# Performance work log

Hardware: AMD Instinct MI355X
Metric: run time of the kernel (lower is better)

Reference implementation:

```python
import jax, jax.numpy as jnp
import numpy as np

B, L, C, H = 16, 680, 1024, 16
PATCH_NUMS = [1, 4, 9, 16, 25, 36, 64, 100, 169, 256]  # per-scale token counts, sum == L
MAX_SCALE_LOG = float(np.log(100.0))


def setup_inputs() -> dict:
    key = jax.random.key(0)
    ks = jax.random.split(key, 4)
    return {
        "x": jax.random.normal(ks[0], (B, L, C), jnp.float32),
        "patch_nums": jnp.asarray(PATCH_NUMS, jnp.int32),
        "mat_qkv_w": (jax.random.normal(ks[1], (3 * C, C), jnp.float32) * 0.02),
        "q_bias": jnp.zeros((C,), jnp.float32),
        "v_bias": jnp.zeros((C,), jnp.float32),
        "scale_log": jnp.full((1, H, 1, 1), np.log(4.0), jnp.float32),
        "proj_w": (jax.random.normal(ks[2], (C, C), jnp.float32) * 0.02),
        "proj_b": jnp.zeros((C,), jnp.float32),
    }


def _l2norm(t):
    # F.normalize(dim=-1): x / max(||x||_2, eps)
    n = jnp.sqrt(jnp.sum(t * t, axis=-1, keepdims=True))
    return t / jnp.maximum(n, 1e-12)


def reference(x, patch_nums, mat_qkv_w, q_bias, v_bias, scale_log, proj_w, proj_b):
    b, l, c = x.shape
    h = scale_log.shape[1]
    d = c // h
    # fused QKV linear with bias = cat(q_bias, zeros, v_bias)
    bias = jnp.concatenate([q_bias, jnp.zeros_like(q_bias), v_bias])
    qkv = (x @ mat_qkv_w.T + bias).reshape(b, l, 3, h, d)
    q, k, v = qkv[:, :, 0], qkv[:, :, 1], qkv[:, :, 2]  # [B, L, H, D]
    # attn_l2_norm path: scale=1, learned per-head multiplier on normalized q
    scale_mul = jnp.exp(jnp.minimum(scale_log, MAX_SCALE_LOG)).transpose(0, 2, 1, 3)  # (1,1,H,1)
    q = _l2norm(q) * scale_mul
    k = _l2norm(k)
    # training path: block-diagonal varlen attention, one block per scale
    pn = np.asarray(patch_nums).tolist()  # static scale schedule
    outs, start = [], 0
    for ln in pn:
        qs = q[:, start:start + ln]
        ks_ = k[:, start:start + ln]
        vs = v[:, start:start + ln]
        s = jnp.einsum("bihd,bjhd->bhij", qs, ks_)  # softmax_scale = 1
        a = jax.nn.softmax(s, axis=-1)
        outs.append(jnp.einsum("bhij,bjhd->bihd", a, vs))
        start += ln
    oup = jnp.concatenate(outs, axis=1).reshape(b, l, c)
    return oup @ proj_w.T + proj_b
```

## Files before the change

### kernel.cpp

```cpp
#include <hip/hip_runtime.h>

typedef __attribute__((ext_vector_type(8))) short bf16x8;
typedef __attribute__((ext_vector_type(4))) float f32x4;

#define Hh   16
#define Ll   680
#define Cc   1024
#define Bb   16
#define NSEG 10
#define LPAD 720

__device__ __forceinline__ unsigned short f32_bf16(float f) {
  union { float f; unsigned int u; } x; x.f = f;
  unsigned int r = x.u + 0x7FFFu + ((x.u >> 16) & 1u);
  return (unsigned short)(r >> 16);
}
__device__ __forceinline__ float bf16_f32(unsigned short u) {
  union { unsigned int u; float f; } x; x.u = ((unsigned int)u) << 16;
  return x.f;
}

__device__ __forceinline__ void async_copy16(const unsigned short* g, unsigned short* l) {
  __builtin_amdgcn_global_load_lds(
      (const __attribute__((address_space(1))) unsigned int*)g,
      (__attribute__((address_space(3))) unsigned int*)l, 16, 0, 0);
}

__device__ __constant__ int c_start2[11] = {0,1,5,14,30,55,91,155,255,424,680};
__device__ __constant__ int c_ps[NSEG]   = {0,8,16,32,48,80,120,184,288,464};
__device__ __constant__ int c_seg[16]    = {0,1,2,3,4,5,6,7,7,8,8,8,9,9,9,9};
__device__ __constant__ int c_tile0[16]  = {0,0,0,0,0,0,0,0,4,0,4,8,0,4,8,12};
__device__ __constant__ int c_len[NSEG]  = {1,4,9,16,25,36,64,100,169,256};

struct PlTab { unsigned short v[Ll]; };
constexpr PlTab make_pl() {
  PlTab t{};
  int starts[11] = {0,1,5,14,30,55,91,155,255,424,680};
  int ps[10]     = {0,8,16,32,48,80,120,184,288,464};
  for (int s = 0; s < 10; ++s)
    for (int l = starts[s]; l < starts[s + 1]; ++l)
      t.v[l] = (unsigned short)(l - starts[s] + ps[s]);
  return t;
}
__device__ __constant__ PlTab c_plt = make_pl();

__global__ __launch_bounds__(256) void conv_kernel(const float* __restrict__ src,
                                                   unsigned short* __restrict__ dst, int n) {
  int i = (blockIdx.x * 256 + threadIdx.x) * 4;
  if (i + 3 < n) {
    float4 v = *reinterpret_cast<const float4*>(src + i);
    ushort4 o;
    o.x = f32_bf16(v.x); o.y = f32_bf16(v.y); o.z = f32_bf16(v.z); o.w = f32_bf16(v.w);
    *reinterpret_cast<ushort4*>(dst + i) = o;
  }
}

__device__ __forceinline__ void stage_ab(const unsigned short* __restrict__ A,
                                         const unsigned short* __restrict__ Bm,
                                         unsigned short* __restrict__ As,
                                         unsigned short* __restrict__ Bs,
                                         int m0, int n0, int k0, int t, int wbase) {
#pragma unroll
  for (int i = 0; i < 2; ++i) {
    int c = i * 512 + t;
    int r = c >> 3;
    int part = (c & 7) ^ (r & 7);
    async_copy16(A + (size_t)(m0 + r) * 1024 + k0 + part * 8,
                 As + (size_t)(i * 512 + wbase) * 8);
  }
#pragma unroll
  for (int i = 0; i < 4; ++i) {
    int c = i * 512 + t;
    int r = c >> 3;
    int part = (c & 7) ^ (r & 7);
    async_copy16(Bm + (size_t)(n0 + r) * 1024 + k0 + part * 8,
                 Bs + (size_t)(i * 512 + wbase) * 8);
  }
}

__global__ __launch_bounds__(512, 2) void gemm_qkv(const unsigned short* __restrict__ A,
                                                   const unsigned short* __restrict__ Bm,
                                                   const float* __restrict__ qb,
                                                   const float* __restrict__ vb,
                                                   unsigned short* __restrict__ qn,
                                                   unsigned short* __restrict__ kn,
                                                   unsigned short* __restrict__ vtb) {
  __shared__ __align__(16) unsigned short lds[2][24576];
  const int t = threadIdx.x;
  const int lane = t & 63, w = t >> 6;
  const int col = lane & 15, quad = lane >> 4;
  const int wm = (w & 1) * 64, wn = (w >> 1) * 64;
  const int m0 = blockIdx.y * 128, n0 = blockIdx.x * 256;
  const int wbase = w * 64;

  f32x4 acc[4][4];
#pragma unroll
  for (int i = 0; i < 4; ++i)
#pragma unroll
    for (int j = 0; j < 4; ++j)
#pragma unroll
      for (int r = 0; r < 4; ++r) acc[i][j][r] = 0.f;

  stage_ab(A, Bm, lds[0], lds[0] + 8192, m0, n0, 0, t, wbase);
  stage_ab(A, Bm, lds[1], lds[1] + 8192, m0, n0, 64, t, wbase);
  asm volatile("s_waitcnt vmcnt(6)" ::: "memory");
  __builtin_amdgcn_s_barrier();
  __builtin_amdgcn_sched_barrier(0);

  for (int tt = 0; tt < 16; ++tt) {
    unsigned short* As = lds[tt & 1];
    unsigned short* Bs = lds[tt & 1] + 8192;
    bf16x8 bf[4][2], af[2][2];

#pragma unroll
    for (int ni = 0; ni < 4; ++ni) {
      int row = wn + ni * 16 + col;
#pragma unroll
      for (int kq = 0; kq < 2; ++kq)
        bf[ni][kq] = *reinterpret_cast<const bf16x8*>(
            &Bs[(row * 8 + ((kq * 4 + quad) ^ (col & 7))) * 8]);
    }
#pragma unroll
    for (int mi = 0; mi < 2; ++mi) {
      int row = wm + mi * 16 + col;
#pragma unroll
      for (int kq = 0; kq < 2; ++kq)
        af[mi][kq] = *reinterpret_cast<const bf16x8*>(
            &As[(row * 8 + ((kq * 4 + quad) ^ (col & 7))) * 8]);
    }
    __builtin_amdgcn_s_setprio(1);
#pragma unroll
    for (int mi = 0; mi < 2; ++mi)
#pragma unroll
      for (int ni = 0; ni < 4; ++ni)
#pragma unroll
        for (int kq = 0; kq < 2; ++kq)
          acc[mi][ni] = __builtin_amdgcn_mfma_f32_16x16x32_bf16(af[mi][kq], bf[ni][kq],
                                                                acc[mi][ni], 0, 0, 0);
    __builtin_amdgcn_s_setprio(0);
    __builtin_amdgcn_s_barrier();

#pragma unroll
    for (int mi = 0; mi < 2; ++mi) {
      int row = wm + (2 + mi) * 16 + col;
#pragma unroll
      for (int kq = 0; kq < 2; ++kq)
        af[mi][kq] = *reinterpret_cast<const bf16x8*>(
            &As[(row * 8 + ((kq * 4 + quad) ^ (col & 7))) * 8]);
    }
    __builtin_amdgcn_s_setprio(1);
#pragma unroll
    for (int mi = 0; mi < 2; ++mi)
#pragma unroll
      for (int ni = 0; ni < 4; ++ni)
#pragma unroll
        for (int kq = 0; kq < 2; ++kq)
          acc[2 + mi][ni] = __builtin_amdgcn_mfma_f32_16x16x32_bf16(af[mi][kq], bf[ni][kq],
                                                                    acc[2 + mi][ni], 0, 0, 0);
    __builtin_amdgcn_s_setprio(0);
    __builtin_amdgcn_s_barrier();

    if (tt < 14) {
      stage_ab(A, Bm, lds[tt & 1], lds[tt & 1] + 8192, m0, n0, (tt + 2) * 64, t, wbase);
      asm volatile("s_waitcnt vmcnt(6)" ::: "memory");
      __builtin_amdgcn_s_barrier();
      __builtin_amdgcn_sched_barrier(0);
    } else if (tt == 14) {
      asm volatile("s_waitcnt vmcnt(0)" ::: "memory");
      __builtin_amdgcn_s_barrier();
      __builtin_amdgcn_sched_barrier(0);
    }
  }

  const int nbase = n0 + wn;
  const int field = nbase >> 10;
  const int h = (nbase >> 6) & 15;

  if (field < 2) {
    float scl[4][4];
    if (field == 1) {
#pragma unroll
      for (int mi = 0; mi < 4; ++mi)
#pragma unroll
        for (int r = 0; r < 4; ++r) {
          float s = 0.f;
#pragma unroll
          for (int ni = 0; ni < 4; ++ni) s += acc[mi][ni][r] * acc[mi][ni][r];
          s += __shfl_xor(s, 1); s += __shfl_xor(s, 2);
          s += __shfl_xor(s, 4); s += __shfl_xor(s, 8);
          scl[mi][r] = 1.f / fmaxf(sqrtf(s), 1e-12f);
        }
    }
    unsigned short* dst0 = (field == 0) ? qn : kn;
#pragma unroll
    for (int ni = 0; ni < 4; ++ni) {
      const int d = ni * 16 + col;
      const float bv = (field == 0) ? qb[h * 64 + d] : 0.f;
#pragma unroll
      for (int mi = 0; mi < 4; ++mi)
#pragma unroll
        for (int r = 0; r < 4; ++r) {
          int gm = m0 + wm + mi * 16 + quad * 4 + r;
          int b = gm / 680, l = gm - b * 680;
          float v = (field == 0) ? (acc[mi][ni][r] + bv) : (acc[mi][ni][r] * scl[mi][r]);
          dst0[((size_t)(b * Hh + h) * Ll + l) * 64 + d] = f32_bf16(v);
        }
    }
  } else {
#pragma unroll
    for (int mi = 0; mi < 4; ++mi) {
      int pl4[4], bb4[4];
#pragma unroll
      for (int r = 0; r < 4; ++r) {
        int gm = m0 + wm + mi * 16 + quad * 4 + r;
        int b = gm / 680, l = gm - b * 680;
        pl4[r] = c_plt.v[l];
        bb4[r] = b;
      }
#pragma unroll
      for (int ni = 0; ni < 4; ++ni) {
        const int d = ni * 16 + col;
        const float bv = vb[h * 64 + d];
#pragma unroll
        for (int r = 0; r < 4; ++r)
          vtb[((size_t)(bb4[r] * Hh + h) * 64 + d) * LPAD + pl4[r]] =
              f32_bf16(acc[mi][ni][r] + bv);
      }
    }
  }
}

__global__ __launch_bounds__(256) void gemm_bt(const unsigned short* __restrict__ A,
                                               const unsigned short* __restrict__ Bm,
                                               const float* __restrict__ bias,
                                               float* __restrict__ outp,
                                               int M, int N, int K) {
  __shared__ __align__(16) unsigned short As[128 * 64];
  __shared__ __align__(16) unsigned short Bs[128 * 64];
  const int t = threadIdx.x;
  const int lane = t & 63, w = t >> 6;
  const int col = lane & 15, quad = lane >> 4;
  const int wm = (w & 1) * 64, wn = (w >> 1) * 64;
  const int m0 = blockIdx.y * 128, n0 = blockIdx.x * 128;

  f32x4 acc[4][4];
#pragma unroll
  for (int i = 0; i < 4; ++i)
#pragma unroll
    for (int j = 0; j < 4; ++j)
#pragma unroll
      for (int r = 0; r < 4; ++r) acc[i][j][r] = 0.f;

  const int cbase = w * 256 + lane;
  for (int k0 = 0; k0 < K; k0 += 64) {
    __syncthreads();
#pragma unroll
    for (int i = 0; i < 4; ++i) {
      int c = cbase + i * 64;
      int r = c >> 3;
      int part = (c & 7) ^ (r & 7);
      async_copy16(A + (size_t)(m0 + r) * K + k0 + part * 8, As + (w * 256 + i * 64) * 8);
      async_copy16(Bm + (size_t)(n0 + r) * K + k0 + part * 8, Bs + (w * 256 + i * 64) * 8);
    }
    __syncthreads();
#pragma unroll
    for (int kk = 0; kk < 64; kk += 32) {
      const int p = (kk >> 3) + quad;
      bf16x8 af[4], bfr[4];
#pragma unroll
      for (int mi = 0; mi < 4; ++mi) {
        int row = wm + mi * 16 + col;
        af[mi] = *reinterpret_cast<const bf16x8*>(&As[(row * 8 + (p ^ (col & 7))) * 8]);
      }
#pragma unroll
      for (int ni = 0; ni < 4; ++ni) {
        int row = wn + ni * 16 + col;
        bfr[ni] = *reinterpret_cast<const bf16x8*>(&Bs[(row * 8 + (p ^ (col & 7))) * 8]);
      }
#pragma unroll
      for (int mi = 0; mi < 4; ++mi)
#pragma unroll
        for (int ni = 0; ni < 4; ++ni)
          acc[mi][ni] = __builtin_amdgcn_mfma_f32_16x16x32_bf16(af[mi], bfr[ni], acc[mi][ni], 0, 0, 0);
    }
  }
#pragma unroll
  for (int mi = 0; mi < 4; ++mi)
#pragma unroll
    for (int ni = 0; ni < 4; ++ni) {
      int gn = n0 + wn + ni * 16 + col;
      float bv = bias[gn];
#pragma unroll
      for (int r = 0; r < 4; ++r) {
        int gm = m0 + wm + mi * 16 + quad * 4 + r;
        outp[(size_t)gm * N + gn] = acc[mi][ni][r] + bv;
      }
    }
}

__global__ __launch_bounds__(256) void attn_kernel(const unsigned short* __restrict__ qn,
                                                   const unsigned short* __restrict__ kn,
                                                   const unsigned short* __restrict__ vtb,
                                                   const float* __restrict__ slog,
                                                   unsigned short* __restrict__ outb) {
  __shared__ __align__(16) unsigned short Ks[128 * 64];
  __shared__ __align__(16) unsigned short Vs[64 * 128];
  __shared__ __align__(16) unsigned short Ps[4 * 16 * 132];

  const int t = threadIdx.x;
  const int lane = t & 63, w = t >> 6;
  const int col = lane & 15, quad = lane >> 4;
  const int wi = blockIdx.x >> 8, bh = blockIdx.x & 255;
  const int h = bh & 15;
  const int seg = c_seg[wi];
  const int start = c_start2[seg], ln = c_len[seg], ps = c_ps[seg];
  const int njt = (ln + 15) >> 4;
  const int nchunk = (njt + 7) >> 3;
  const int qt = c_tile0[wi] + w;
  const bool qvalid = qt < njt;
  const float smul = __expf(fminf(slog[h], 4.6051701859880914f));

  const int qi = qt * 16 + col;
  const unsigned short* qrow = qn + ((size_t)bh * Ll + start + qi) * 64;
  bf16x8 qf0 = *reinterpret_cast<const bf16x8*>(qrow + quad * 8);
  bf16x8 qf1 = *reinterpret_cast<const bf16x8*>(qrow + 32 + quad * 8);
  {
    float ss = 0.f;
#pragma unroll
    for (int e = 0; e < 8; ++e) {
      float f0 = bf16_f32((unsigned short)qf0[e]), f1 = bf16_f32((unsigned short)qf1[e]);
      ss += f0 * f0 + f1 * f1;
    }
    ss += __shfl_xor(ss, 16);
    ss += __shfl_xor(ss, 32);
    const float qsc = smul / fmaxf(sqrtf(ss), 1e-12f);
#pragma unroll
    for (int e = 0; e < 8; ++e) {
      qf0[e] = (short)f32_bf16(bf16_f32((unsigned short)qf0[e]) * qsc);
      qf1[e] = (short)f32_bf16(bf16_f32((unsigned short)qf1[e]) * qsc);
    }
  }

  f32x4 o[4];
#pragma unroll
  for (int nt = 0; nt < 4; ++nt)
#pragma unroll
    for (int r = 0; r < 4; ++r) o[nt][r] = 0.f;
  float m4[4] = {-1e30f, -1e30f, -1e30f, -1e30f};
  float l4[4] = {0.f, 0.f, 0.f, 0.f};

  const int jc_t = (t & 15) ^ (t >> 4);

  for (int ch = 0; ch < nchunk; ++ch) {
    const int jbase = ch * 128;
    const int jtc = (njt - ch * 8 > 8) ? 8 : (njt - ch * 8);
    const int jtcp = (jtc + 1) & ~1;
    const int rowsK = jtc * 16;
    const int jcmax = jtcp * 2;
    __syncthreads();

#pragma unroll
    for (int i = 0; i < 4; ++i) {
      int c = i * 256 + w * 64 + lane;
      int jr = c >> 3;
      if (jr < rowsK) {
        int cc = (c & 7) ^ (jr & 7);
        async_copy16(kn + ((size_t)bh * Ll + start + jbase + jr) * 64 + cc * 8,
                     Ks + (i * 256 + w * 64) * 8);
      }
    }
    if (jc_t < jcmax) {
#pragma unroll
      for (int i = 0; i < 4; ++i) {
        int d = i * 16 + (t >> 4);
        async_copy16(vtb + ((size_t)bh * 64 + d) * LPAD + ps + jbase + jc_t * 8,
                     Vs + (i * 256 + w * 64) * 8);
      }
    }
    __syncthreads();

    f32x4 sf[8];
#pragma unroll
    for (int jt = 0; jt < 8; ++jt) {
      if (jt >= jtcp) continue;
      f32x4 s;
#pragma unroll
      for (int r = 0; r < 4; ++r) s[r] = 0.f;
      if (jt < jtc) {
        int jrow = jt * 16 + col;
        bf16x8 k0 = *reinterpret_cast<const bf16x8*>(&Ks[(jrow * 8 + (quad ^ (jrow & 7))) * 8]);
        bf16x8 k1 = *reinterpret_cast<const bf16x8*>(&Ks[(jrow * 8 + ((4 + quad) ^ (jrow & 7))) * 8]);
        s = __builtin_amdgcn_mfma_f32_16x16x32_bf16(qf0, k0, s, 0, 0, 0);
        s = __builtin_amdgcn_mfma_f32_16x16x32_bf16(qf1, k1, s, 0, 0, 0);
      }
      if (jbase + jt * 16 + col >= ln) {
#pragma unroll
        for (int r = 0; r < 4; ++r) s[r] = -1e30f;
      }
      sf[jt] = s;
    }
    float mc[4];
#pragma unroll
    for (int r = 0; r < 4; ++r) mc[r] = sf[0][r];
#pragma unroll
    for (int jt = 1; jt < 8; ++jt) {
      if (jt >= jtcp) continue;
#pragma unroll
      for (int r = 0; r < 4; ++r) mc[r] = fmaxf(mc[r], sf[jt][r]);
    }
#pragma unroll
    for (int mask = 1; mask <= 8; mask <<= 1)
#pragma unroll
      for (int r = 0; r < 4; ++r) mc[r] = fmaxf(mc[r], __shfl_xor(mc[r], mask));
    float alpha[4];
#pragma unroll
    for (int r = 0; r < 4; ++r) {
      float mn = fmaxf(m4[r], mc[r]);
      alpha[r] = __expf(m4[r] - mn);
      m4[r] = mn;
    }
    float ls[4] = {0.f, 0.f, 0.f, 0.f};
#pragma unroll
    for (int jt = 0; jt < 8; ++jt) {
      if (jt >= jtcp) continue;
#pragma unroll
      for (int r = 0; r < 4; ++r) {
        float pv = __expf(sf[jt][r] - m4[r]);
        ls[r] += pv;
        Ps[(w * 16 + quad * 4 + r) * 132 + jt * 16 + col] = f32_bf16(pv);
      }
    }
#pragma unroll
    for (int mask = 1; mask <= 8; mask <<= 1)
#pragma unroll
      for (int r = 0; r < 4; ++r) ls[r] += __shfl_xor(ls[r], mask);
#pragma unroll
    for (int r = 0; r < 4; ++r) l4[r] = l4[r] * alpha[r] + ls[r];
#pragma unroll
    for (int nt = 0; nt < 4; ++nt)
#pragma unroll
      for (int r = 0; r < 4; ++r) o[nt][r] *= alpha[r];

#pragma unroll
    for (int kk2 = 0; kk2 < 4; ++kk2) {
      if (kk2 >= (jtcp >> 1)) continue;
      bf16x8 pf = *reinterpret_cast<const bf16x8*>(&Ps[(w * 16 + col) * 132 + kk2 * 32 + quad * 8]);
#pragma unroll
      for (int nt = 0; nt < 4; ++nt) {
        int d = nt * 16 + col;
        int slot = (kk2 * 4 + quad) ^ (d & 15);
        bf16x8 vf = *reinterpret_cast<const bf16x8*>(&Vs[(d * 16 + slot) * 8]);
        o[nt] = __builtin_amdgcn_mfma_f32_16x16x32_bf16(pf, vf, o[nt], 0, 0, 0);
      }
    }
  }

  if (qvalid) {
    float inv[4];
#pragma unroll
    for (int r = 0; r < 4; ++r) inv[r] = 1.f / l4[r];
    const int b = bh >> 4;
#pragma unroll
    for (int nt = 0; nt < 4; ++nt)
#pragma unroll
      for (int r = 0; r < 4; ++r) {
        int ri = qt * 16 + quad * 4 + r;
        if (ri < ln) {
          size_t off = ((size_t)b * Ll + start + ri) * Cc + h * 64 + nt * 16 + col;
          outb[off] = f32_bf16(o[nt][r] * inv[r]);
        }
      }
  }
}

extern "C" void kernel_launch(void* const* d_in, const int* in_sizes, int n_in,
                              void* d_out, int out_size, void* d_ws, size_t ws_size,
                              hipStream_t stream) {
  const float* x     = (const float*)d_in[0];
  const float* wqkv  = (const float*)d_in[2];
  const float* qbias = (const float*)d_in[3];
  const float* vbias = (const float*)d_in[4];
  const float* slog  = (const float*)d_in[5];
  const float* wproj = (const float*)d_in[6];
  const float* pbias = (const float*)d_in[7];
  float* out = (float*)d_out;

  const size_t nX  = (size_t)Bb * Ll * Cc;
  const size_t nWq = (size_t)3 * Cc * Cc;
  const size_t nWp = (size_t)Cc * Cc;
  const size_t nVt = (size_t)Bb * Hh * 64 * LPAD;

  char* p = (char*)d_ws;
  unsigned short* xb     = (unsigned short*)p;  p += nX * 2;
  unsigned short* wqkvb  = (unsigned short*)p;  p += nWq * 2;
  unsigned short* wprojb = (unsigned short*)p;  p += nWp * 2;
  unsigned short* qn     = (unsigned short*)p;  p += nX * 2;
  unsigned short* kn     = (unsigned short*)p;  p += nX * 2;
  unsigned short* vtb    = (unsigned short*)p;  p += nVt * 2;
  unsigned short* attn   = xb;

  conv_kernel<<<(int)(nX / 1024), 256, 0, stream>>>(x, xb, (int)nX);
  conv_kernel<<<(int)(nWq / 1024), 256, 0, stream>>>(wqkv, wqkvb, (int)nWq);
  conv_kernel<<<(int)(nWp / 1024), 256, 0, stream>>>(wproj, wprojb, (int)nWp);

  gemm_qkv<<<dim3(12, 85), 512, 0, stream>>>(xb, wqkvb, qbias, vbias, qn, kn, vtb);
  attn_kernel<<<Bb * Hh * 16, 256, 0, stream>>>(qn, kn, vtb, slog, attn);
  gemm_bt<<<dim3(8, 85), 256, 0, stream>>>(attn, wprojb, pbias, out, 10880, 1024, 1024);
}
```

Baseline: 333.0 us.

## Triple-buffer QKV GEMM with half-tile staging interleaved between MFMA phases

Reworks the QKV GEMM main loop from two whole-tile LDS buffers to three buffers split into halves. Each half is prefetched between the two MFMA phases, two to three k-steps ahead, and the waitcnt levels are adjusted to match. The per-wave row mapping changes so each wave works on 32-row slices of each A half, and the epilogue row index is updated to that mapping. The goal is to keep global loads in flight across the MFMA work and avoid the stall at the end of each iteration. The cost is more LDS per block (144KB instead of 96KB, which may limit occupancy at two blocks per CU), extra barriers, and clamped redundant loads past the last k-step.

```diff
diff --git a/kernel.cpp b/kernel.cpp
--- a/kernel.cpp
+++ b/kernel.cpp
@@ -55,29 +55,6 @@
   }
 }
 
-__device__ __forceinline__ void stage_ab(const unsigned short* __restrict__ A,
-                                         const unsigned short* __restrict__ Bm,
-                                         unsigned short* __restrict__ As,
-                                         unsigned short* __restrict__ Bs,
-                                         int m0, int n0, int k0, int t, int wbase) {
-#pragma unroll
-  for (int i = 0; i < 2; ++i) {
-    int c = i * 512 + t;
-    int r = c >> 3;
-    int part = (c & 7) ^ (r & 7);
-    async_copy16(A + (size_t)(m0 + r) * 1024 + k0 + part * 8,
-                 As + (size_t)(i * 512 + wbase) * 8);
-  }
-#pragma unroll
-  for (int i = 0; i < 4; ++i) {
-    int c = i * 512 + t;
-    int r = c >> 3;
-    int part = (c & 7) ^ (r & 7);
-    async_copy16(Bm + (size_t)(n0 + r) * 1024 + k0 + part * 8,
-                 Bs + (size_t)(i * 512 + wbase) * 8);
-  }
-}
-
 __global__ __launch_bounds__(512, 2) void gemm_qkv(const unsigned short* __restrict__ A,
                                                    const unsigned short* __restrict__ Bm,
                                                    const float* __restrict__ qb,
@@ -85,13 +62,32 @@
                                                    unsigned short* __restrict__ qn,
                                                    unsigned short* __restrict__ kn,
                                                    unsigned short* __restrict__ vtb) {
-  __shared__ __align__(16) unsigned short lds[2][24576];
+  __shared__ __align__(16) unsigned short lds[73728];
   const int t = threadIdx.x;
   const int lane = t & 63, w = t >> 6;
   const int col = lane & 15, quad = lane >> 4;
-  const int wm = (w & 1) * 64, wn = (w >> 1) * 64;
+  const int wn = (w >> 1) * 64;
   const int m0 = blockIdx.y * 128, n0 = blockIdx.x * 256;
-  const int wbase = w * 64;
+  const int bhs = wn >> 7;
+
+  auto stageA = [&](int d3, int hs, int k0) {
+    int kc = k0 > 960 ? 960 : k0;
+    int r = t >> 3;
+    int part = (t & 7) ^ (r & 7);
+    async_copy16(A + (size_t)(m0 + hs * 64 + r) * 1024 + kc + part * 8,
+                 lds + (d3 * 2 + hs) * 4096 + w * 512);
+  };
+  auto stageB = [&](int d3, int hs, int k0) {
+    int kc = k0 > 960 ? 960 : k0;
+#pragma unroll
+    for (int i = 0; i < 2; ++i) {
+      int c = i * 512 + t;
+      int r = c >> 3;
+      int part = (c & 7) ^ (r & 7);
+      async_copy16(Bm + (size_t)(n0 + hs * 128 + r) * 1024 + kc + part * 8,
+                   lds + 24576 + (d3 * 2 + hs) * 8192 + (i * 512 + w * 64) * 8);
+    }
+  };
 
   f32x4 acc[4][4];
 #pragma unroll
@@ -101,75 +97,86 @@
 #pragma unroll
       for (int r = 0; r < 4; ++r) acc[i][j][r] = 0.f;
 
-  stage_ab(A, Bm, lds[0], lds[0] + 8192, m0, n0, 0, t, wbase);
-  stage_ab(A, Bm, lds[1], lds[1] + 8192, m0, n0, 64, t, wbase);
-  asm volatile("s_waitcnt vmcnt(6)" ::: "memory");
+#pragma unroll
+  for (int tt = 0; tt < 2; ++tt) {
+    stageB(tt, 0, tt * 64); stageA(tt, 0, tt * 64);
+    stageB(tt, 1, tt * 64); stageA(tt, 1, tt * 64);
+  }
+  stageB(2, 0, 128); stageA(2, 0, 128);
+  asm volatile("s_waitcnt vmcnt(9)" ::: "memory");
   __builtin_amdgcn_s_barrier();
   __builtin_amdgcn_sched_barrier(0);
 
+  int bsel = 0;
   for (int tt = 0; tt < 16; ++tt) {
-    unsigned short* As = lds[tt & 1];
-    unsigned short* Bs = lds[tt & 1] + 8192;
-    bf16x8 bf[4][2], af[2][2];
-
-#pragma unroll
-    for (int ni = 0; ni < 4; ++ni) {
-      int row = wn + ni * 16 + col;
+    const int b  = bsel;
+    const int b2 = (bsel + 2 >= 3) ? bsel - 1 : bsel + 2;
+    const unsigned short* As0 = lds + (b * 2 + 0) * 4096;
+    const unsigned short* As1 = lds + (b * 2 + 1) * 4096;
+    const unsigned short* Bs  = lds + 24576 + (b * 2 + bhs) * 8192;
+    bf16x8 bfr[4][2], af[2][2];
+
+#pragma unroll
+    for (int nf = 0; nf < 4; ++nf) {
+      int rb = (wn & 64) + nf * 16 + col;
 #pragma unroll
       for (int kq = 0; kq < 2; ++kq)
-        bf[ni][kq] = *reinterpret_cast<const bf16x8*>(
-            &Bs[(row * 8 + ((kq * 4 + quad) ^ (col & 7))) * 8]);
-    }
-#pragma unroll
-    for (int mi = 0; mi < 2; ++mi) {
-      int row = wm + mi * 16 + col;
+        bfr[nf][kq] = *reinterpret_cast<const bf16x8*>(
+            &Bs[(rb * 8 + ((kq * 4 + quad) ^ (col & 7))) * 8]);
+    }
+#pragma unroll
+    for (int j = 0; j < 2; ++j) {
+      int ri = (w & 1) * 32 + j * 16 + col;
 #pragma unroll
       for (int kq = 0; kq < 2; ++kq)
-        af[mi][kq] = *reinterpret_cast<const bf16x8*>(
-            &As[(row * 8 + ((kq * 4 + quad) ^ (col & 7))) * 8]);
-    }
+        af[j][kq] = *reinterpret_cast<const bf16x8*>(
+            &As0[(ri * 8 + ((kq * 4 + quad) ^ (col & 7))) * 8]);
+    }
+    stageB(b2, 1, (tt + 2) * 64);
+    stageA(b2, 1, (tt + 2) * 64);
+    __builtin_amdgcn_s_barrier();
     __builtin_amdgcn_s_setprio(1);
 #pragma unroll
-    for (int mi = 0; mi < 2; ++mi)
-#pragma unroll
-      for (int ni = 0; ni < 4; ++ni)
+    for (int j = 0; j < 2; ++j)
+#pragma unroll
+      for (int nf = 0; nf < 4; ++nf)
 #pragma unroll
         for (int kq = 0; kq < 2; ++kq)
-          acc[mi][ni] = __builtin_amdgcn_mfma_f32_16x16x32_bf16(af[mi][kq], bf[ni][kq],
-                                                                acc[mi][ni], 0, 0, 0);
+          acc[j][nf] = __builtin_amdgcn_mfma_f32_16x16x32_bf16(af[j][kq], bfr[nf][kq],
+                                                               acc[j][nf], 0, 0, 0);
     __builtin_amdgcn_s_setprio(0);
+    __builtin_amdgcn_sched_barrier(0);
+    asm volatile("s_waitcnt vmcnt(6)" ::: "memory");
     __builtin_amdgcn_s_barrier();
-
-#pragma unroll
-    for (int mi = 0; mi < 2; ++mi) {
-      int row = wm + (2 + mi) * 16 + col;
+    __builtin_amdgcn_sched_barrier(0);
+
+#pragma unroll
+    for (int j = 0; j < 2; ++j) {
+      int ri = (w & 1) * 32 + j * 16 + col;
 #pragma unroll
       for (int kq = 0; kq < 2; ++kq)
-        af[mi][kq] = *reinterpret_cast<const bf16x8*>(
-            &As[(row * 8 + ((kq * 4 + quad) ^ (col & 7))) * 8]);
-    }
+        af[j][kq] = *reinterpret_cast<const bf16x8*>(
+            &As1[(ri * 8 + ((kq * 4 + quad) ^ (col & 7))) * 8]);
+    }
+    stageB(b, 0, (tt + 3) * 64);
+    stageA(b, 0, (tt + 3) * 64);
+    __builtin_amdgcn_s_barrier();
     __builtin_amdgcn_s_setprio(1);
 #pragma unroll
-    for (int mi = 0; mi < 2; ++mi)
-#pragma unroll
-      for (int ni = 0; ni < 4; ++ni)
+    for (int j = 0; j < 2; ++j)
+#pragma unroll
+      for (int nf = 0; nf < 4; ++nf)
 #pragma unroll
         for (int kq = 0; kq < 2; ++kq)
-          acc[2 + mi][ni] = __builtin_amdgcn_mfma_f32_16x16x32_bf16(af[mi][kq], bf[ni][kq],
-                                                                    acc[2 + mi][ni], 0, 0, 0);
+          acc[2 + j][nf] = __builtin_amdgcn_mfma_f32_16x16x32_bf16(af[j][kq], bfr[nf][kq],
+                                                                   acc[2 + j][nf], 0, 0, 0);
     __builtin_amdgcn_s_setprio(0);
+    __builtin_amdgcn_sched_barrier(0);
+    asm volatile("s_waitcnt vmcnt(9)" ::: "memory");
     __builtin_amdgcn_s_barrier();
-
-    if (tt < 14) {
-      stage_ab(A, Bm, lds[tt & 1], lds[tt & 1] + 8192, m0, n0, (tt + 2) * 64, t, wbase);
-      asm volatile("s_waitcnt vmcnt(6)" ::: "memory");
-      __builtin_amdgcn_s_barrier();
-      __builtin_amdgcn_sched_barrier(0);
-    } else if (tt == 14) {
-      asm volatile("s_waitcnt vmcnt(0)" ::: "memory");
-      __builtin_amdgcn_s_barrier();
-      __builtin_amdgcn_sched_barrier(0);
-    }
+    __builtin_amdgcn_sched_barrier(0);
+
+    bsel = (bsel == 2) ? 0 : bsel + 1;
   }
 
   const int nbase = n0 + wn;
@@ -200,7 +207,7 @@
       for (int mi = 0; mi < 4; ++mi)
 #pragma unroll
         for (int r = 0; r < 4; ++r) {
-          int gm = m0 + wm + mi * 16 + quad * 4 + r;
+          int gm = m0 + (mi >> 1) * 64 + (w & 1) * 32 + (mi & 1) * 16 + quad * 4 + r;
           int b = gm / 680, l = gm - b * 680;
           float v = (field == 0) ? (acc[mi][ni][r] + bv) : (acc[mi][ni][r] * scl[mi][r]);
           dst0[((size_t)(b * Hh + h) * Ll + l) * 64 + d] = f32_bf16(v);
@@ -212,7 +219,7 @@
       int pl4[4], bb4[4];
 #pragma unroll
       for (int r = 0; r < 4; ++r) {
-        int gm = m0 + wm + mi * 16 + quad * 4 + r;
+        int gm = m0 + (mi >> 1) * 64 + (w & 1) * 32 + (mi & 1) * 16 + quad * 4 + r;
         int b = gm / 680, l = gm - b * 680;
         pl4[r] = c_plt.v[l];
         bb4[r] = b;
```

Result: faster. 323.1 us (-3.0%).
